# Kernel optimization log

Measured on AMD Instinct MI355X. Metric: run time of the kernel, lower is better.

Reference implementation:

```python
import jax, jax.numpy as jnp
import numpy as np

B, N, C = 256, 196, 256
RES, RES_, STRIDE = 14, 7, 2
H, KD, D = 16, 16, 64          # heads, key_dim, d=attn_ratio*key_dim
NH_KD, DH = H * KD, H * D      # 256, 1024
HW = DH + NH_KD                # kv width 1280
OUT = 512
EPS = 1e-5
SCALE = KD ** -0.5


def make_bias_idxs():
    pts = [(i, j) for i in range(RES) for j in range(RES)]
    pts_ = [(i, j) for i in range(RES_) for j in range(RES_)]
    offsets, idxs = {}, []
    for p1 in pts_:
        for p2 in pts:
            off = (abs(p1[0] * STRIDE - p2[0]), abs(p1[1] * STRIDE - p2[1]))
            if off not in offsets:
                offsets[off] = len(offsets)
            idxs.append(offsets[off])
    return np.array(idxs, np.int32).reshape(len(pts_), len(pts)), len(offsets)


def bn(x, g, b, m, v):
    return (x - m) * (g / jnp.sqrt(v + EPS)) + b


def hardswish(x):
    return x * jnp.clip(x + 3.0, 0.0, 6.0) / 6.0


def setup_inputs() -> dict:
    key = jax.random.key(0)
    ks = jax.random.split(key, 12)
    idxs, n_off = make_bias_idxs()
    s_in, s_dh = (2.0 / C) ** 0.5, (2.0 / DH) ** 0.5
    return {
        "x": jax.random.normal(ks[0], (B, N, C), jnp.float32),
        "W_kv": jax.random.normal(ks[1], (HW, C), jnp.float32) * s_in,
        "g_kv": jnp.ones((HW,)), "b_kv": jnp.zeros((HW,)),
        "m_kv": jax.random.normal(ks[2], (HW,)) * 0.1,
        "v_kv": jax.random.uniform(ks[3], (HW,), minval=0.5, maxval=1.5),
        "W_q": jax.random.normal(ks[4], (NH_KD, C), jnp.float32) * s_in,
        "g_q": jnp.ones((NH_KD,)), "b_q": jnp.zeros((NH_KD,)),
        "m_q": jax.random.normal(ks[5], (NH_KD,)) * 0.1,
        "v_q": jax.random.uniform(ks[6], (NH_KD,), minval=0.5, maxval=1.5),
        "W_p": jax.random.normal(ks[7], (OUT, DH), jnp.float32) * s_dh,
        "g_p": jnp.ones((OUT,)), "b_p": jnp.zeros((OUT,)),
        "m_p": jax.random.normal(ks[8], (OUT,)) * 0.1,
        "v_p": jax.random.uniform(ks[9], (OUT,), minval=0.5, maxval=1.5),
        "attn_biases": jax.random.normal(ks[10], (H, n_off), jnp.float32) * 0.02,
        "bias_idxs": jnp.asarray(idxs),
    }


def reference(x, W_kv, g_kv, b_kv, m_kv, v_kv, W_q, g_q, b_q, m_q, v_q,
              W_p, g_p, b_p, m_p, v_p, attn_biases, bias_idxs):
    # kv branch: Linear(no bias) + BN over flattened tokens
    kv = bn(jnp.einsum('bnc,hc->bnh', x, W_kv), g_kv, b_kv, m_kv, v_kv)
    kv = kv.reshape(B, N, H, KD + D)
    k, v = kv[..., :KD], kv[..., KD:]                 # [B,N,H,KD], [B,N,H,D]
    # q branch: spatial subsample stride 2 then LinearNorm
    xs = x.reshape(B, RES, RES, C)[:, ::STRIDE, ::STRIDE].reshape(B, RES_ * RES_, C)
    q = bn(jnp.einsum('bnc,hc->bnh', xs, W_q), g_q, b_q, m_q, v_q)
    q = q.reshape(B, RES_ * RES_, H, KD)              # [B,49,H,KD]
    bias = attn_biases[:, bias_idxs]                  # [H,49,196]
    attn = jnp.einsum('bqhd,bkhd->bhqk', q, k) * SCALE + bias
    attn = jax.nn.softmax(attn, axis=-1)
    o = jnp.einsum('bhqk,bkhd->bqhd', attn, v).reshape(B, RES_ * RES_, DH)
    return bn(jnp.einsum('bnd,od->bno', hardswish(o), W_p), g_p, b_p, m_p, v_p)
```

## Files before the change

kernel.cpp:

```cpp
#include <hip/hip_runtime.h>

typedef unsigned short u16;
typedef unsigned int u32;
typedef __attribute__((ext_vector_type(8))) short bf16x8;
typedef __attribute__((ext_vector_type(4))) float f32x4;

__device__ __forceinline__ u16 f2bf(float x) {
  union { float f; u32 u; } un; un.f = x;
  u32 r = un.u + 0x7FFFu + ((un.u >> 16) & 1u);
  return (u16)(r >> 16);
}

__device__ __forceinline__ void gl_lds16(const u16* gsrc, u16* ldst) {
  __builtin_amdgcn_global_load_lds(
      (const __attribute__((address_space(1))) void*)gsrc,
      (__attribute__((address_space(3))) void*)ldst,
      16, 0, 0);
}

__global__ __launch_bounds__(256) void prep_misc(
    const float* __restrict__ Wkv, const float* __restrict__ Wq, const float* __restrict__ Wp,
    const float* __restrict__ gkv, const float* __restrict__ bkv, const float* __restrict__ mkv, const float* __restrict__ vkv,
    const float* __restrict__ gq, const float* __restrict__ bq, const float* __restrict__ mq, const float* __restrict__ vq,
    const float* __restrict__ gp, const float* __restrict__ bp, const float* __restrict__ mp, const float* __restrict__ vp,
    const float* __restrict__ ab, const int* __restrict__ bidx,
    u16* __restrict__ wkvb, u16* __restrict__ wqb, u16* __restrict__ wpb,
    float* __restrict__ skv, float* __restrict__ tkv,
    float* __restrict__ sq, float* __restrict__ tq,
    float* __restrict__ sp, float* __restrict__ tp,
    float* __restrict__ biasf)
{
  int i = blockIdx.x * 256 + threadIdx.x;
  if (i < 327680) { wkvb[i] = f2bf(Wkv[i]); return; }
  i -= 327680;
  if (i < 65536) { wqb[i] = f2bf(Wq[i]); return; }
  i -= 65536;
  if (i < 524288) { wpb[i] = f2bf(Wp[i]); return; }
  i -= 524288;
  if (i < 153664) { biasf[i] = ab[(i / 9604) * 196 + bidx[i % 9604]]; return; }
  i -= 153664;
  if (i < 1280) { float s = gkv[i] * rsqrtf(vkv[i] + 1e-5f); skv[i] = s; tkv[i] = bkv[i] - mkv[i] * s; return; }
  i -= 1280;
  if (i < 256) {
    int h = i >> 4, c = i & 15;
    float sk = gkv[h * 80 + c] * rsqrtf(vkv[h * 80 + c] + 1e-5f);
    float s = gq[i] * rsqrtf(vq[i] + 1e-5f);
    sq[i] = s * 0.25f * sk;
    tq[i] = (bq[i] - mq[i] * s) * 0.25f * sk;
    return;
  }
  i -= 256;
  if (i < 512) { float s = gp[i] * rsqrtf(vp[i] + 1e-5f); sp[i] = s; tp[i] = bp[i] - mp[i] * s; return; }
}

__global__ __launch_bounds__(256) void conv_x(const float* __restrict__ x, u16* __restrict__ xb)
{
  int u = blockIdx.x * 256 + threadIdx.x;
  float4 v = ((const float4*)x)[u];
  uint2 o;
  o.x = (u32)f2bf(v.x) | ((u32)f2bf(v.y) << 16);
  o.y = (u32)f2bf(v.z) | ((u32)f2bf(v.w) << 16);
  ((uint2*)xb)[u] = o;
}

__global__ __launch_bounds__(256) void gemm_bn(
    const u16* __restrict__ A, const u16* __restrict__ W,
    const float* __restrict__ sv, const float* __restrict__ tv,
    float* __restrict__ outp, int N, int K, int NBLK)
{
  __shared__ u16 As[128 * 64];
  __shared__ u16 Bs[128 * 64];
  const int tid = threadIdx.x;
  const int lane = tid & 63;
  const int wv = tid >> 6, wr = wv >> 1, wc = wv & 1;
  const int lo = lane & 15, hi = lane >> 4;

  int bid = blockIdx.x;
  int cpx = gridDim.x >> 3;
  int wg = (bid & 7) * cpx + (bid >> 3);
  const int m0 = (wg / NBLK) * 128, n0 = (wg % NBLK) * 128;

  f32x4 zero4 = {0.f, 0.f, 0.f, 0.f};
  f32x4 acc[4][4];
#pragma unroll
  for (int m = 0; m < 4; ++m)
#pragma unroll
    for (int n = 0; n < 4; ++n) acc[m][n] = zero4;

  for (int kt = 0; kt < K; kt += 64) {
    __syncthreads();
#pragma unroll
    for (int i = 0; i < 4; ++i) {
      int e = (i * 256 + tid) * 8;
      int r = e >> 6, c = e & 63;
      int cs = c ^ ((r & 7) << 3);
      gl_lds16(A + (long)(m0 + r) * K + (kt + cs), As + e);
      gl_lds16(W + (long)(n0 + r) * K + (kt + cs), Bs + e);
    }
    __syncthreads();
#pragma unroll
    for (int kk = 0; kk < 64; kk += 32) {
      bf16x8 af[4], bfr[4];
#pragma unroll
      for (int m = 0; m < 4; ++m)
        af[m] = *(const bf16x8*)(As + (wr * 64 + m * 16 + lo) * 64 + ((kk + hi * 8) ^ ((lo & 7) << 3)));
#pragma unroll
      for (int n = 0; n < 4; ++n)
        bfr[n] = *(const bf16x8*)(Bs + (wc * 64 + n * 16 + lo) * 64 + ((kk + hi * 8) ^ ((lo & 7) << 3)));
#pragma unroll
      for (int m = 0; m < 4; ++m)
#pragma unroll
        for (int n = 0; n < 4; ++n)
          acc[m][n] = __builtin_amdgcn_mfma_f32_16x16x32_bf16(af[m], bfr[n], acc[m][n], 0, 0, 0);
    }
  }
#pragma unroll
  for (int m = 0; m < 4; ++m) {
    const int row0 = m0 + wr * 64 + m * 16 + hi * 4;
#pragma unroll
    for (int n = 0; n < 4; ++n) {
      const int col = n0 + wc * 64 + n * 16 + lo;
      const float s = sv[col], t = tv[col];
#pragma unroll
      for (int j = 0; j < 4; ++j)
        outp[(long)(row0 + j) * N + col] = acc[m][n][j] * s + t;
    }
  }
}

#define VTS   208
#define KOFF  13312
#define KS    24
#define QOFF  18304
#define QS    24
#define POFF  13312
#define PS    208
#define SMEM_N 26624

__device__ __forceinline__ int swz(int col, int rowkey) {
  return (col < 192) ? (col ^ ((rowkey & 7) << 3)) : col;
}

__global__ __launch_bounds__(256, 3) void fused_attn(
    const u16* __restrict__ xb, const u16* __restrict__ wkvb, const u16* __restrict__ wqb,
    const float* __restrict__ skv, const float* __restrict__ tkv,
    const float* __restrict__ sqv, const float* __restrict__ tqv,
    const float* __restrict__ biasf, u16* __restrict__ osw)
{
  __shared__ __align__(16) u16 sm[SMEM_N];
  const int tid = threadIdx.x;
  const int bid = blockIdx.x;
  const int wg = (bid & 7) * 512 + (bid >> 3);
  const int bb = wg >> 4, hh = wg & 15;
  const int w = tid >> 6, lane = tid & 63, lo = lane & 15, hi = lane >> 4;

  const u16* xbase = xb + (long)bb * 196 * 256;
  const u16* wkvh = wkvb + (long)hh * 80 * 256;
  const u16* wqh  = wqb + (long)hh * 16 * 256;

  f32x4 z4 = {0.f, 0.f, 0.f, 0.f};
  f32x4 acc[3][5];
#pragma unroll
  for (int u = 0; u < 3; ++u)
#pragma unroll
    for (int nf = 0; nf < 5; ++nf) acc[u][nf] = z4;
  f32x4 acc12a = z4, acc12b = z4;
  f32x4 qacc = z4;

  int qi = w * 16 + lo; if (qi > 48) qi = 48;
  const int gr = (qi / 7) * 28 + (qi % 7) * 2;

  const int kx = ((lo >> 1) & 3) << 3;
  const int kq = ((gr >> 1) & 3) << 3;

  auto stage = [&](int t) {
    const int kt = t * 32;
    u16* xbuf = sm + (t & 1) * 6656;
    u16* wbuf = sm + 13312 + (t & 1) * 3072;
#pragma unroll
    for (int i = 0; i < 4; ++i) {
      int idx = i * 256 + tid;
      if (idx < 832) {
        int e = idx * 8;
        int r = e >> 5, c = e & 31;
        int xr = (r < 196) ? r : 195;
        int cs = c ^ (((r >> 1) & 3) << 3);
        gl_lds16(xbase + (long)xr * 256 + kt + cs, xbuf + e);
      }
    }
#pragma unroll
    for (int i = 0; i < 2; ++i) {
      int idx = i * 256 + tid;
      if (idx < 384) {
        int e = idx * 8;
        int r = e >> 5, c = e & 31;
        int cs = c ^ (((r >> 1) & 3) << 3);
        const u16* src = (r < 80) ? (wkvh + (long)r * 256 + kt + cs)
                                  : (wqh + (long)(r - 80) * 256 + kt + cs);
        gl_lds16(src, wbuf + e);
      }
    }
  };

  stage(0);
  __syncthreads();
#pragma unroll
  for (int t = 0; t < 8; ++t) {
    if (t < 7) stage(t + 1);
    const u16* xbuf = sm + (t & 1) * 6656;
    const u16* wbuf = sm + 13312 + (t & 1) * 3072;
    const int ra = hi * 8;
    __builtin_amdgcn_s_setprio(1);
    {
      bf16x8 bfr[6];
#pragma unroll
      for (int nf = 0; nf < 6; ++nf)
        bfr[nf] = *(const bf16x8*)(wbuf + (nf * 16 + lo) * 32 + (ra ^ kx));
      {
        bf16x8 aqf = *(const bf16x8*)(xbuf + gr * 32 + (ra ^ kq));
        qacc = __builtin_amdgcn_mfma_f32_16x16x32_bf16(aqf, bfr[5], qacc, 0, 0, 0);
      }
#pragma unroll
      for (int u = 0; u < 3; ++u) {
        bf16x8 af = *(const bf16x8*)(xbuf + ((w + u * 4) * 16 + lo) * 32 + (ra ^ kx));
#pragma unroll
        for (int nf = 0; nf < 5; ++nf)
          acc[u][nf] = __builtin_amdgcn_mfma_f32_16x16x32_bf16(af, bfr[nf], acc[u][nf], 0, 0, 0);
      }
      if (w) {
        bf16x8 af12 = *(const bf16x8*)(xbuf + (192 + lo) * 32 + (ra ^ kx));
        if (w == 1) {
          acc12a = __builtin_amdgcn_mfma_f32_16x16x32_bf16(af12, bfr[0], acc12a, 0, 0, 0);
          acc12b = __builtin_amdgcn_mfma_f32_16x16x32_bf16(af12, bfr[1], acc12b, 0, 0, 0);
        } else if (w == 2) {
          acc12a = __builtin_amdgcn_mfma_f32_16x16x32_bf16(af12, bfr[2], acc12a, 0, 0, 0);
          acc12b = __builtin_amdgcn_mfma_f32_16x16x32_bf16(af12, bfr[3], acc12b, 0, 0, 0);
        } else {
          acc12a = __builtin_amdgcn_mfma_f32_16x16x32_bf16(af12, bfr[4], acc12a, 0, 0, 0);
        }
      }
    }
    __builtin_amdgcn_s_setprio(0);
    __syncthreads();
  }

#pragma unroll
  for (int u = 0; u < 3; ++u) {
    const int mf = w + u * 4;
    const int nnb = mf * 16 + hi * 4;
#pragma unroll
    for (int j = 0; j < 4; ++j)
      sm[KOFF + (nnb + j) * KS + lo] = f2bf(acc[u][0][j]);
#pragma unroll
    for (int nf = 1; nf < 5; ++nf) {
      const int d = nf * 16 - 16 + lo;
      uint2 pp;
      pp.x = (u32)f2bf(acc[u][nf][0]) | ((u32)f2bf(acc[u][nf][1]) << 16);
      pp.y = (u32)f2bf(acc[u][nf][2]) | ((u32)f2bf(acc[u][nf][3]) << 16);
      *(uint2*)(sm + d * VTS + swz(nnb, d)) = pp;
    }
  }
  {
    const int nnb = 192 + hi * 4;
    if (w == 1) {
#pragma unroll
      for (int j = 0; j < 4; ++j)
        sm[KOFF + (nnb + j) * KS + lo] = f2bf(acc12a[j]);
      const int d = lo;
      uint2 pp;
      pp.x = (u32)f2bf(acc12b[0]) | ((u32)f2bf(acc12b[1]) << 16);
      pp.y = (u32)f2bf(acc12b[2]) | ((u32)f2bf(acc12b[3]) << 16);
      *(uint2*)(sm + d * VTS + swz(nnb, d)) = pp;
    } else if (w == 2) {
      const int d0 = 16 + lo, d1 = 32 + lo;
      uint2 pa, pb;
      pa.x = (u32)f2bf(acc12a[0]) | ((u32)f2bf(acc12a[1]) << 16);
      pa.y = (u32)f2bf(acc12a[2]) | ((u32)f2bf(acc12a[3]) << 16);
      pb.x = (u32)f2bf(acc12b[0]) | ((u32)f2bf(acc12b[1]) << 16);
      pb.y = (u32)f2bf(acc12b[2]) | ((u32)f2bf(acc12b[3]) << 16);
      *(uint2*)(sm + d0 * VTS + swz(nnb, d0)) = pa;
      *(uint2*)(sm + d1 * VTS + swz(nnb, d1)) = pb;
    } else if (w == 3) {
      const int d = 48 + lo;
      uint2 pp;
      pp.x = (u32)f2bf(acc12a[0]) | ((u32)f2bf(acc12a[1]) << 16);
      pp.y = (u32)f2bf(acc12a[2]) | ((u32)f2bf(acc12a[3]) << 16);
      *(uint2*)(sm + d * VTS + swz(nnb, d)) = pp;
    }
  }
  {
    const float s = sqv[hh * 16 + lo], t = tqv[hh * 16 + lo];
#pragma unroll
    for (int j = 0; j < 4; ++j) {
      const int r = w * 16 + hi * 4 + j;
      sm[QOFF + r * QS + lo] = f2bf(qacc[j] * s + t);
    }
  }
  __syncthreads();

  f32x4 sc[13];
  {
    bf16x8 zf = {0, 0, 0, 0, 0, 0, 0, 0};
    bf16x8 aq2 = zf;
    if (hi < 2) aq2 = *(const bf16x8*)(sm + QOFF + (w * 16 + lo) * QS + hi * 8);
#pragma unroll
    for (int t13 = 0; t13 < 13; ++t13) {
      bf16x8 bk = zf;
      if (hi < 2) bk = *(const bf16x8*)(sm + KOFF + (t13 * 16 + lo) * KS + hi * 8);
      sc[t13] = __builtin_amdgcn_mfma_f32_16x16x32_bf16(aq2, bk, z4, 0, 0, 0);
    }
  }
  __syncthreads();

  float rs[4];
#pragma unroll
  for (int j = 0; j < 4; ++j) {
    const int row = w * 16 + hi * 4 + j;
    const int rb = (row < 49) ? row : 0;
    float vals[13];
#pragma unroll
    for (int t = 0; t < 13; ++t) {
      const int col = t * 16 + lo;
      vals[t] = (col < 196) ? sc[t][j] + biasf[(hh * 49 + rb) * 196 + col] : -1e30f;
    }
    float mx = vals[0];
#pragma unroll
    for (int t = 1; t < 13; ++t) mx = fmaxf(mx, vals[t]);
#pragma unroll
    for (int s = 1; s < 16; s <<= 1) mx = fmaxf(mx, __shfl_xor(mx, s, 64));
    float sum = 0.f;
#pragma unroll
    for (int t = 0; t < 13; ++t) { float p = __expf(vals[t] - mx); vals[t] = p; sum += p; }
#pragma unroll
    for (int s = 1; s < 16; s <<= 1) sum += __shfl_xor(sum, s, 64);
#pragma unroll
    for (int t = 0; t < 13; ++t) sm[POFF + row * PS + swz(t * 16 + lo, row)] = f2bf(vals[t]);
    rs[j] = sum;
  }

  f32x4 oacc[4];
#pragma unroll
  for (int n = 0; n < 4; ++n) oacc[n] = z4;
  __builtin_amdgcn_s_setprio(1);
#pragma unroll
  for (int kt = 0; kt < 192; kt += 32) {
    bf16x8 ap = *(const bf16x8*)(sm + POFF + (w * 16 + lo) * PS + ((kt + hi * 8) ^ ((lo & 7) << 3)));
#pragma unroll
    for (int n = 0; n < 4; ++n) {
      bf16x8 bv = *(const bf16x8*)(sm + (n * 16 + lo) * VTS + ((kt + hi * 8) ^ ((lo & 7) << 3)));
      oacc[n] = __builtin_amdgcn_mfma_f32_16x16x32_bf16(ap, bv, oacc[n], 0, 0, 0);
    }
  }
  {
    bf16x8 zf = {0, 0, 0, 0, 0, 0, 0, 0};
    bf16x8 ap = zf;
    if (hi < 2) ap = *(const bf16x8*)(sm + POFF + (w * 16 + lo) * PS + 192 + hi * 8);
#pragma unroll
    for (int n = 0; n < 4; ++n) {
      bf16x8 bv = zf;
      if (hi < 2) bv = *(const bf16x8*)(sm + (n * 16 + lo) * VTS + 192 + hi * 8);
      oacc[n] = __builtin_amdgcn_mfma_f32_16x16x32_bf16(ap, bv, oacc[n], 0, 0, 0);
    }
  }
  __builtin_amdgcn_s_setprio(0);

  float svv[4], tvv[4];
#pragma unroll
  for (int n = 0; n < 4; ++n) {
    svv[n] = skv[hh * 80 + 16 + n * 16 + lo];
    tvv[n] = tkv[hh * 80 + 16 + n * 16 + lo];
  }
#pragma unroll
  for (int j = 0; j < 4; ++j) {
    const int row = w * 16 + hi * 4 + j;
    if (row < 49) {
      const float rinv = 1.f / rs[j];
      const long ob = ((long)(bb * 49 + row)) * 1024 + hh * 64 + lo;
#pragma unroll
      for (int n = 0; n < 4; ++n) {
        float val = oacc[n][j] * svv[n] * rinv + tvv[n];
        float hs = val * fminf(fmaxf(val + 3.f, 0.f), 6.f) * (1.f / 6.f);
        osw[ob + n * 16] = f2bf(hs);
      }
    }
  }
}

extern "C" void kernel_launch(void* const* d_in, const int* in_sizes, int n_in,
                              void* d_out, int out_size, void* d_ws, size_t ws_size,
                              hipStream_t stream)
{
  const float* x   = (const float*)d_in[0];
  const float* Wkv = (const float*)d_in[1];
  const float* gkv = (const float*)d_in[2];
  const float* bkv = (const float*)d_in[3];
  const float* mkv = (const float*)d_in[4];
  const float* vkv = (const float*)d_in[5];
  const float* Wq  = (const float*)d_in[6];
  const float* gq  = (const float*)d_in[7];
  const float* bq  = (const float*)d_in[8];
  const float* mq  = (const float*)d_in[9];
  const float* vq  = (const float*)d_in[10];
  const float* Wp  = (const float*)d_in[11];
  const float* gp  = (const float*)d_in[12];
  const float* bp  = (const float*)d_in[13];
  const float* mp  = (const float*)d_in[14];
  const float* vp  = (const float*)d_in[15];
  const float* ab  = (const float*)d_in[16];
  const int* bidx  = (const int*)d_in[17];

  char* ws = (char*)d_ws;
  size_t off = 0;
  auto alloc = [&](size_t bytes) -> char* {
    char* p = ws + off;
    off += (bytes + 255) & ~(size_t)255;
    return p;
  };
  u16* x_bf   = (u16*)alloc((size_t)50176 * 256 * 2);
  u16* wkv_bf = (u16*)alloc((size_t)1280 * 256 * 2);
  u16* wq_bf  = (u16*)alloc((size_t)256 * 256 * 2);
  u16* wp_bf  = (u16*)alloc((size_t)512 * 1024 * 2);
  u16* hsw    = (u16*)alloc((size_t)12544 * 1024 * 2);
  float* bias_f = (float*)alloc((size_t)153664 * 4);
  float* s_kv = (float*)alloc(1280 * 4);
  float* t_kv = (float*)alloc(1280 * 4);
  float* s_q  = (float*)alloc(256 * 4);
  float* t_q  = (float*)alloc(256 * 4);
  float* s_p  = (float*)alloc(512 * 4);
  float* t_p  = (float*)alloc(512 * 4);
  if (off > ws_size) return;

  prep_misc<<<4193, 256, 0, stream>>>(Wkv, Wq, Wp, gkv, bkv, mkv, vkv,
                                      gq, bq, mq, vq, gp, bp, mp, vp,
                                      ab, bidx, wkv_bf, wq_bf, wp_bf,
                                      s_kv, t_kv, s_q, t_q, s_p, t_p, bias_f);
  conv_x<<<12544, 256, 0, stream>>>(x, x_bf);
  fused_attn<<<4096, 256, 0, stream>>>(x_bf, wkv_bf, wq_bf, s_kv, t_kv, s_q, t_q, bias_f, hsw);
  gemm_bn<<<392, 256, 0, stream>>>(hsw, wp_bf, s_p, t_p, (float*)d_out, 512, 1024, 4);
}
```

Before: 125.8 us.

## Keep softmax probabilities in registers via transposed MFMA and lane shuffles

The QK^T MFMA operands are swapped so each lane owns one query row, which turns the softmax reductions into two cross-lane shuffles. The probabilities are then repacked into PV MFMA operands with lane shuffles instead of a round trip through shared memory. This removes the P buffer from LDS, shrinks shared memory, drops a barrier, and raises the occupancy hint from 3 to 4 blocks. The output epilogue also switches to vectorized 8-byte stores and float4 loads for the bias and scale. The cost is extra shuffle and select instructions, plus higher register pressure under the tighter launch bound.

Result: slower. 137.8 us (+9.6%).

```diff
diff --git a/kernel.cpp b/kernel.cpp
--- a/kernel.cpp
+++ b/kernel.cpp
@@ -9,6 +9,9 @@
   union { float f; u32 u; } un; un.f = x;
   u32 r = un.u + 0x7FFFu + ((un.u >> 16) & 1u);
   return (u16)(r >> 16);
+}
+__device__ __forceinline__ u32 pk2(float a, float b) {
+  return (u32)f2bf(a) | ((u32)f2bf(b) << 16);
 }
 
 __device__ __forceinline__ void gl_lds16(const u16* gsrc, u16* ldst) {
@@ -133,15 +136,13 @@
 #define KS    24
 #define QOFF  18304
 #define QS    24
-#define POFF  13312
-#define PS    208
-#define SMEM_N 26624
+#define SMEM_N 19840
 
 __device__ __forceinline__ int swz(int col, int rowkey) {
   return (col < 192) ? (col ^ ((rowkey & 7) << 3)) : col;
 }
 
-__global__ __launch_bounds__(256, 3) void fused_attn(
+__global__ __launch_bounds__(256, 4) void fused_attn(
     const u16* __restrict__ xb, const u16* __restrict__ wkvb, const u16* __restrict__ wqb,
     const float* __restrict__ skv, const float* __restrict__ tkv,
     const float* __restrict__ sqv, const float* __restrict__ tqv,
@@ -255,8 +256,8 @@
     for (int nf = 1; nf < 5; ++nf) {
       const int d = nf * 16 - 16 + lo;
       uint2 pp;
-      pp.x = (u32)f2bf(acc[u][nf][0]) | ((u32)f2bf(acc[u][nf][1]) << 16);
-      pp.y = (u32)f2bf(acc[u][nf][2]) | ((u32)f2bf(acc[u][nf][3]) << 16);
+      pp.x = pk2(acc[u][nf][0], acc[u][nf][1]);
+      pp.y = pk2(acc[u][nf][2], acc[u][nf][3]);
       *(uint2*)(sm + d * VTS + swz(nnb, d)) = pp;
     }
   }
@@ -268,23 +269,23 @@
         sm[KOFF + (nnb + j) * KS + lo] = f2bf(acc12a[j]);
       const int d = lo;
       uint2 pp;
-      pp.x = (u32)f2bf(acc12b[0]) | ((u32)f2bf(acc12b[1]) << 16);
-      pp.y = (u32)f2bf(acc12b[2]) | ((u32)f2bf(acc12b[3]) << 16);
+      pp.x = pk2(acc12b[0], acc12b[1]);
+      pp.y = pk2(acc12b[2], acc12b[3]);
       *(uint2*)(sm + d * VTS + swz(nnb, d)) = pp;
     } else if (w == 2) {
       const int d0 = 16 + lo, d1 = 32 + lo;
       uint2 pa, pb;
-      pa.x = (u32)f2bf(acc12a[0]) | ((u32)f2bf(acc12a[1]) << 16);
-      pa.y = (u32)f2bf(acc12a[2]) | ((u32)f2bf(acc12a[3]) << 16);
-      pb.x = (u32)f2bf(acc12b[0]) | ((u32)f2bf(acc12b[1]) << 16);
-      pb.y = (u32)f2bf(acc12b[2]) | ((u32)f2bf(acc12b[3]) << 16);
+      pa.x = pk2(acc12a[0], acc12a[1]);
+      pa.y = pk2(acc12a[2], acc12a[3]);
+      pb.x = pk2(acc12b[0], acc12b[1]);
+      pb.y = pk2(acc12b[2], acc12b[3]);
       *(uint2*)(sm + d0 * VTS + swz(nnb, d0)) = pa;
       *(uint2*)(sm + d1 * VTS + swz(nnb, d1)) = pb;
     } else if (w == 3) {
       const int d = 48 + lo;
       uint2 pp;
-      pp.x = (u32)f2bf(acc12a[0]) | ((u32)f2bf(acc12a[1]) << 16);
-      pp.y = (u32)f2bf(acc12a[2]) | ((u32)f2bf(acc12a[3]) << 16);
+      pp.x = pk2(acc12a[0], acc12a[1]);
+      pp.y = pk2(acc12a[2], acc12a[3]);
       *(uint2*)(sm + d * VTS + swz(nnb, d)) = pp;
     }
   }
@@ -307,81 +308,101 @@
     for (int t13 = 0; t13 < 13; ++t13) {
       bf16x8 bk = zf;
       if (hi < 2) bk = *(const bf16x8*)(sm + KOFF + (t13 * 16 + lo) * KS + hi * 8);
-      sc[t13] = __builtin_amdgcn_mfma_f32_16x16x32_bf16(aq2, bk, z4, 0, 0, 0);
-    }
-  }
-  __syncthreads();
-
-  float rs[4];
-#pragma unroll
-  for (int j = 0; j < 4; ++j) {
-    const int row = w * 16 + hi * 4 + j;
-    const int rb = (row < 49) ? row : 0;
-    float vals[13];
-#pragma unroll
-    for (int t = 0; t < 13; ++t) {
-      const int col = t * 16 + lo;
-      vals[t] = (col < 196) ? sc[t][j] + biasf[(hh * 49 + rb) * 196 + col] : -1e30f;
-    }
-    float mx = vals[0];
-#pragma unroll
-    for (int t = 1; t < 13; ++t) mx = fmaxf(mx, vals[t]);
-#pragma unroll
-    for (int s = 1; s < 16; s <<= 1) mx = fmaxf(mx, __shfl_xor(mx, s, 64));
-    float sum = 0.f;
-#pragma unroll
-    for (int t = 0; t < 13; ++t) { float p = __expf(vals[t] - mx); vals[t] = p; sum += p; }
-#pragma unroll
-    for (int s = 1; s < 16; s <<= 1) sum += __shfl_xor(sum, s, 64);
-#pragma unroll
-    for (int t = 0; t < 13; ++t) sm[POFF + row * PS + swz(t * 16 + lo, row)] = f2bf(vals[t]);
-    rs[j] = sum;
-  }
+      sc[t13] = __builtin_amdgcn_mfma_f32_16x16x32_bf16(bk, aq2, z4, 0, 0, 0);
+    }
+  }
+
+  const int q = w * 16 + lo;
+  const int rb = (q < 49) ? q : 48;
+  const float* bptr = biasf + (long)(hh * 49 + rb) * 196;
+  float mx = -1e30f;
+#pragma unroll
+  for (int t = 0; t < 13; ++t) {
+    float4 b4 = *(const float4*)(bptr + t * 16 + hi * 4);
+    f32x4 v = sc[t];
+    v[0] += b4.x; v[1] += b4.y; v[2] += b4.z; v[3] += b4.w;
+    if (t == 12) {
+      if (hi != 0) { v[0] = -1e30f; v[1] = -1e30f; v[2] = -1e30f; v[3] = -1e30f; }
+    }
+    sc[t] = v;
+    mx = fmaxf(mx, fmaxf(fmaxf(v[0], v[1]), fmaxf(v[2], v[3])));
+  }
+  mx = fmaxf(mx, __shfl_xor(mx, 16, 64));
+  mx = fmaxf(mx, __shfl_xor(mx, 32, 64));
+  float sum = 0.f;
+#pragma unroll
+  for (int t = 0; t < 13; ++t) {
+    f32x4 v = sc[t];
+#pragma unroll
+    for (int j = 0; j < 4; ++j) { float p = __expf(v[j] - mx); v[j] = p; sum += p; }
+    sc[t] = v;
+  }
+  sum += __shfl_xor(sum, 16, 64);
+  sum += __shfl_xor(sum, 32, 64);
 
   f32x4 oacc[4];
 #pragma unroll
   for (int n = 0; n < 4; ++n) oacc[n] = z4;
+  const int s1 = lo + ((hi & 1) << 5);
+  const bool selB = (hi >> 1) != 0;
   __builtin_amdgcn_s_setprio(1);
 #pragma unroll
-  for (int kt = 0; kt < 192; kt += 32) {
-    bf16x8 ap = *(const bf16x8*)(sm + POFF + (w * 16 + lo) * PS + ((kt + hi * 8) ^ ((lo & 7) << 3)));
+  for (int c = 0; c < 7; ++c) {
+    const int kt = c * 32;
+    u32 a0 = pk2(sc[2 * c][0], sc[2 * c][1]);
+    u32 a1 = pk2(sc[2 * c][2], sc[2 * c][3]);
+    u32 b0 = 0, b1 = 0;
+    if (c < 6) {
+      b0 = pk2(sc[2 * c + 1][0], sc[2 * c + 1][1]);
+      b1 = pk2(sc[2 * c + 1][2], sc[2 * c + 1][3]);
+    }
+    u32 A0 = (u32)__shfl((int)a0, s1, 64), A1 = (u32)__shfl((int)a1, s1, 64);
+    u32 B0 = (u32)__shfl((int)b0, s1, 64), B1 = (u32)__shfl((int)b1, s1, 64);
+    u32 A2 = (u32)__shfl((int)a0, s1 + 16, 64), A3 = (u32)__shfl((int)a1, s1 + 16, 64);
+    u32 B2 = (u32)__shfl((int)b0, s1 + 16, 64), B3 = (u32)__shfl((int)b1, s1 + 16, 64);
+    union { u32 u[4]; bf16x8 v; } pf;
+    pf.u[0] = selB ? B0 : A0;
+    pf.u[1] = selB ? B1 : A1;
+    pf.u[2] = selB ? B2 : A2;
+    pf.u[3] = selB ? B3 : A3;
+    if (c < 6) {
+#pragma unroll
+      for (int n = 0; n < 4; ++n) {
+        bf16x8 bv = *(const bf16x8*)(sm + (n * 16 + lo) * VTS + ((kt + hi * 8) ^ ((lo & 7) << 3)));
+        oacc[n] = __builtin_amdgcn_mfma_f32_16x16x32_bf16(bv, pf.v, oacc[n], 0, 0, 0);
+      }
+    } else {
+      bf16x8 zf = {0, 0, 0, 0, 0, 0, 0, 0};
+#pragma unroll
+      for (int n = 0; n < 4; ++n) {
+        bf16x8 bv = zf;
+        if (hi < 2) bv = *(const bf16x8*)(sm + (n * 16 + lo) * VTS + 192 + hi * 8);
+        oacc[n] = __builtin_amdgcn_mfma_f32_16x16x32_bf16(bv, pf.v, oacc[n], 0, 0, 0);
+      }
+    }
+  }
+  __builtin_amdgcn_s_setprio(0);
+
+  if (q < 49) {
+    const float rinv = 1.f / sum;
+    const long ob = ((long)(bb * 49 + q)) * 1024 + hh * 64;
 #pragma unroll
     for (int n = 0; n < 4; ++n) {
-      bf16x8 bv = *(const bf16x8*)(sm + (n * 16 + lo) * VTS + ((kt + hi * 8) ^ ((lo & 7) << 3)));
-      oacc[n] = __builtin_amdgcn_mfma_f32_16x16x32_bf16(ap, bv, oacc[n], 0, 0, 0);
-    }
-  }
-  {
-    bf16x8 zf = {0, 0, 0, 0, 0, 0, 0, 0};
-    bf16x8 ap = zf;
-    if (hi < 2) ap = *(const bf16x8*)(sm + POFF + (w * 16 + lo) * PS + 192 + hi * 8);
-#pragma unroll
-    for (int n = 0; n < 4; ++n) {
-      bf16x8 bv = zf;
-      if (hi < 2) bv = *(const bf16x8*)(sm + (n * 16 + lo) * VTS + 192 + hi * 8);
-      oacc[n] = __builtin_amdgcn_mfma_f32_16x16x32_bf16(ap, bv, oacc[n], 0, 0, 0);
-    }
-  }
-  __builtin_amdgcn_s_setprio(0);
-
-  float svv[4], tvv[4];
-#pragma unroll
-  for (int n = 0; n < 4; ++n) {
-    svv[n] = skv[hh * 80 + 16 + n * 16 + lo];
-    tvv[n] = tkv[hh * 80 + 16 + n * 16 + lo];
-  }
-#pragma unroll
-  for (int j = 0; j < 4; ++j) {
-    const int row = w * 16 + hi * 4 + j;
-    if (row < 49) {
-      const float rinv = 1.f / rs[j];
-      const long ob = ((long)(bb * 49 + row)) * 1024 + hh * 64 + lo;
-#pragma unroll
-      for (int n = 0; n < 4; ++n) {
-        float val = oacc[n][j] * svv[n] * rinv + tvv[n];
-        float hs = val * fminf(fmaxf(val + 3.f, 0.f), 6.f) * (1.f / 6.f);
-        osw[ob + n * 16] = f2bf(hs);
-      }
+      const int d0 = n * 16 + hi * 4;
+      float4 s4 = *(const float4*)(skv + hh * 80 + 16 + d0);
+      float4 t4 = *(const float4*)(tkv + hh * 80 + 16 + d0);
+      float hv[4];
+      hv[0] = oacc[n][0] * s4.x * rinv + t4.x;
+      hv[1] = oacc[n][1] * s4.y * rinv + t4.y;
+      hv[2] = oacc[n][2] * s4.z * rinv + t4.z;
+      hv[3] = oacc[n][3] * s4.w * rinv + t4.w;
+#pragma unroll
+      for (int j = 0; j < 4; ++j)
+        hv[j] = hv[j] * fminf(fmaxf(hv[j] + 3.f, 0.f), 6.f) * (1.f / 6.f);
+      uint2 pp;
+      pp.x = pk2(hv[0], hv[1]);
+      pp.y = pk2(hv[2], hv[3]);
+      *(uint2*)(osw + ob + d0) = pp;
     }
   }
 }
@@ -421,7 +442,7 @@
   u16* wq_bf  = (u16*)alloc((size_t)256 * 256 * 2);
   u16* wp_bf  = (u16*)alloc((size_t)512 * 1024 * 2);
   u16* hsw    = (u16*)alloc((size_t)12544 * 1024 * 2);
-  float* bias_f = (float*)alloc((size_t)153664 * 4);
+  float* bias_f = (float*)alloc((size_t)153664 * 4 + 256);
   float* s_kv = (float*)alloc(1280 * 4);
   float* t_kv = (float*)alloc(1280 * 4);
   float* s_q  = (float*)alloc(256 * 4);
```

## Fuse fp32-to-bf16 conversion of x into attention kernel staging

Applied to the files above, without the earlier changes.

Removes the separate conv_x pass and makes fused_attn read fp32 x directly. Tiles go into registers and are converted with v_cvt_pk_bf16_f32 before the swizzled LDS write, which happens after the MFMA work of each step. This avoids writing and re-reading a bf16 copy of x and saves one launch. In exchange, each of the 16 head blocks per batch reads twice the bytes of x and holds extra registers for the staged loads. It also changes the async global-to-LDS copy into a register round trip.

Result: slower. 130.0 us (+3.4%).

```diff
diff --git a/kernel.cpp b/kernel.cpp
--- a/kernel.cpp
+++ b/kernel.cpp
@@ -9,6 +9,14 @@
   union { float f; u32 u; } un; un.f = x;
   u32 r = un.u + 0x7FFFu + ((un.u >> 16) & 1u);
   return (u16)(r >> 16);
+}
+__device__ __forceinline__ u32 pk2(float a, float b) {
+  return (u32)f2bf(a) | ((u32)f2bf(b) << 16);
+}
+__device__ __forceinline__ u32 cvtpk(float a, float b) {
+  u32 r;
+  asm("v_cvt_pk_bf16_f32 %0, %1, %2" : "=v"(r) : "v"(a), "v"(b));
+  return r;
 }
 
 __device__ __forceinline__ void gl_lds16(const u16* gsrc, u16* ldst) {
@@ -53,16 +61,6 @@
   if (i < 512) { float s = gp[i] * rsqrtf(vp[i] + 1e-5f); sp[i] = s; tp[i] = bp[i] - mp[i] * s; return; }
 }
 
-__global__ __launch_bounds__(256) void conv_x(const float* __restrict__ x, u16* __restrict__ xb)
-{
-  int u = blockIdx.x * 256 + threadIdx.x;
-  float4 v = ((const float4*)x)[u];
-  uint2 o;
-  o.x = (u32)f2bf(v.x) | ((u32)f2bf(v.y) << 16);
-  o.y = (u32)f2bf(v.z) | ((u32)f2bf(v.w) << 16);
-  ((uint2*)xb)[u] = o;
-}
-
 __global__ __launch_bounds__(256) void gemm_bn(
     const u16* __restrict__ A, const u16* __restrict__ W,
     const float* __restrict__ sv, const float* __restrict__ tv,
@@ -142,7 +140,7 @@
 }
 
 __global__ __launch_bounds__(256, 3) void fused_attn(
-    const u16* __restrict__ xb, const u16* __restrict__ wkvb, const u16* __restrict__ wqb,
+    const float* __restrict__ xf32, const u16* __restrict__ wkvb, const u16* __restrict__ wqb,
     const float* __restrict__ skv, const float* __restrict__ tkv,
     const float* __restrict__ sqv, const float* __restrict__ tqv,
     const float* __restrict__ biasf, u16* __restrict__ osw)
@@ -154,7 +152,7 @@
   const int bb = wg >> 4, hh = wg & 15;
   const int w = tid >> 6, lane = tid & 63, lo = lane & 15, hi = lane >> 4;
 
-  const u16* xbase = xb + (long)bb * 196 * 256;
+  const float* xbase = xf32 + (long)bb * 196 * 256;
   const u16* wkvh = wkvb + (long)hh * 80 * 256;
   const u16* wqh  = wqb + (long)hh * 16 * 256;
 
@@ -173,21 +171,41 @@
   const int kx = ((lo >> 1) & 3) << 3;
   const int kq = ((gr >> 1) & 3) << 3;
 
-  auto stage = [&](int t) {
+  float4 lx[4][2];
+  auto load_x = [&](int t) {
     const int kt = t * 32;
-    u16* xbuf = sm + (t & 1) * 6656;
-    u16* wbuf = sm + 13312 + (t & 1) * 3072;
 #pragma unroll
     for (int i = 0; i < 4; ++i) {
       int idx = i * 256 + tid;
       if (idx < 832) {
-        int e = idx * 8;
-        int r = e >> 5, c = e & 31;
+        int r = idx >> 2, c8 = (idx & 3) * 8;
         int xr = (r < 196) ? r : 195;
-        int cs = c ^ (((r >> 1) & 3) << 3);
-        gl_lds16(xbase + (long)xr * 256 + kt + cs, xbuf + e);
-      }
-    }
+        const float* src = xbase + (long)xr * 256 + kt + c8;
+        lx[i][0] = *(const float4*)(src);
+        lx[i][1] = *(const float4*)(src + 4);
+      }
+    }
+  };
+  auto write_x = [&](int t) {
+    u16* xbuf = sm + (t & 1) * 6656;
+#pragma unroll
+    for (int i = 0; i < 4; ++i) {
+      int idx = i * 256 + tid;
+      if (idx < 832) {
+        int r = idx >> 2, c8 = (idx & 3) * 8;
+        int key = ((r >> 1) & 3) << 3;
+        uint4 o;
+        o.x = cvtpk(lx[i][0].x, lx[i][0].y);
+        o.y = cvtpk(lx[i][0].z, lx[i][0].w);
+        o.z = cvtpk(lx[i][1].x, lx[i][1].y);
+        o.w = cvtpk(lx[i][1].z, lx[i][1].w);
+        *(uint4*)(xbuf + r * 32 + (c8 ^ key)) = o;
+      }
+    }
+  };
+  auto stage_w = [&](int t) {
+    const int kt = t * 32;
+    u16* wbuf = sm + 13312 + (t & 1) * 3072;
 #pragma unroll
     for (int i = 0; i < 2; ++i) {
       int idx = i * 256 + tid;
@@ -202,11 +220,13 @@
     }
   };
 
-  stage(0);
+  load_x(0);
+  stage_w(0);
+  write_x(0);
   __syncthreads();
 #pragma unroll
   for (int t = 0; t < 8; ++t) {
-    if (t < 7) stage(t + 1);
+    if (t < 7) { load_x(t + 1); stage_w(t + 1); }
     const u16* xbuf = sm + (t & 1) * 6656;
     const u16* wbuf = sm + 13312 + (t & 1) * 3072;
     const int ra = hi * 8;
@@ -241,6 +261,8 @@
       }
     }
     __builtin_amdgcn_s_setprio(0);
+    __builtin_amdgcn_sched_barrier(0);
+    if (t < 7) write_x(t + 1);
     __syncthreads();
   }
 
@@ -255,8 +277,8 @@
     for (int nf = 1; nf < 5; ++nf) {
       const int d = nf * 16 - 16 + lo;
       uint2 pp;
-      pp.x = (u32)f2bf(acc[u][nf][0]) | ((u32)f2bf(acc[u][nf][1]) << 16);
-      pp.y = (u32)f2bf(acc[u][nf][2]) | ((u32)f2bf(acc[u][nf][3]) << 16);
+      pp.x = pk2(acc[u][nf][0], acc[u][nf][1]);
+      pp.y = pk2(acc[u][nf][2], acc[u][nf][3]);
       *(uint2*)(sm + d * VTS + swz(nnb, d)) = pp;
     }
   }
@@ -268,23 +290,23 @@
         sm[KOFF + (nnb + j) * KS + lo] = f2bf(acc12a[j]);
       const int d = lo;
       uint2 pp;
-      pp.x = (u32)f2bf(acc12b[0]) | ((u32)f2bf(acc12b[1]) << 16);
-      pp.y = (u32)f2bf(acc12b[2]) | ((u32)f2bf(acc12b[3]) << 16);
+      pp.x = pk2(acc12b[0], acc12b[1]);
+      pp.y = pk2(acc12b[2], acc12b[3]);
       *(uint2*)(sm + d * VTS + swz(nnb, d)) = pp;
     } else if (w == 2) {
       const int d0 = 16 + lo, d1 = 32 + lo;
       uint2 pa, pb;
-      pa.x = (u32)f2bf(acc12a[0]) | ((u32)f2bf(acc12a[1]) << 16);
-      pa.y = (u32)f2bf(acc12a[2]) | ((u32)f2bf(acc12a[3]) << 16);
-      pb.x = (u32)f2bf(acc12b[0]) | ((u32)f2bf(acc12b[1]) << 16);
-      pb.y = (u32)f2bf(acc12b[2]) | ((u32)f2bf(acc12b[3]) << 16);
+      pa.x = pk2(acc12a[0], acc12a[1]);
+      pa.y = pk2(acc12a[2], acc12a[3]);
+      pb.x = pk2(acc12b[0], acc12b[1]);
+      pb.y = pk2(acc12b[2], acc12b[3]);
       *(uint2*)(sm + d0 * VTS + swz(nnb, d0)) = pa;
       *(uint2*)(sm + d1 * VTS + swz(nnb, d1)) = pb;
     } else if (w == 3) {
       const int d = 48 + lo;
       uint2 pp;
-      pp.x = (u32)f2bf(acc12a[0]) | ((u32)f2bf(acc12a[1]) << 16);
-      pp.y = (u32)f2bf(acc12a[2]) | ((u32)f2bf(acc12a[3]) << 16);
+      pp.x = pk2(acc12a[0], acc12a[1]);
+      pp.y = pk2(acc12a[2], acc12a[3]);
       *(uint2*)(sm + d * VTS + swz(nnb, d)) = pp;
     }
   }
@@ -416,7 +438,6 @@
     off += (bytes + 255) & ~(size_t)255;
     return p;
   };
-  u16* x_bf   = (u16*)alloc((size_t)50176 * 256 * 2);
   u16* wkv_bf = (u16*)alloc((size_t)1280 * 256 * 2);
   u16* wq_bf  = (u16*)alloc((size_t)256 * 256 * 2);
   u16* wp_bf  = (u16*)alloc((size_t)512 * 1024 * 2);
@@ -434,7 +455,6 @@
                                       gq, bq, mq, vq, gp, bp, mp, vp,
                                       ab, bidx, wkv_bf, wq_bf, wp_bf,
                                       s_kv, t_kv, s_q, t_q, s_p, t_p, bias_f);
-  conv_x<<<12544, 256, 0, stream>>>(x, x_bf);
-  fused_attn<<<4096, 256, 0, stream>>>(x_bf, wkv_bf, wq_bf, s_kv, t_kv, s_q, t_q, bias_f, hsw);
+  fused_attn<<<4096, 256, 0, stream>>>(x, wkv_bf, wq_bf, s_kv, t_kv, s_q, t_q, bias_f, hsw);
   gemm_bn<<<392, 256, 0, stream>>>(hsw, wp_bf, s_p, t_p, (float*)d_out, 512, 1024, 4);
 }
```
